# Optimization experiments

Hardware: AMD Instinct MI355X
Metric: run time of the kernel (lower is better)

The kernel has to match this reference:

```python
import jax, jax.numpy as jnp
import numpy as np

B, T, D, K = 16, 8192, 64, 1024


def setup_inputs() -> dict:
    key = jax.random.key(0)
    k1, k2 = jax.random.split(key)
    x = jax.random.normal(k1, (B, T, D, 1), dtype=jnp.float32)
    weight = jax.random.normal(k2, (K, D), dtype=jnp.float32)
    return {"x": x, "weight": weight}


def reference(x, weight):
    # x: [B, T, D, 1] -> squeeze trailing dim -> [B, T, D]
    xs = jnp.squeeze(x, axis=-1)
    x2 = jnp.sum(xs * xs, axis=-1, keepdims=True)          # [B, T, 1]
    e2 = jnp.sum(weight * weight, axis=-1)                 # [K]
    xe = jnp.einsum('btd,kd->btk', xs, weight)             # [B, T, K]
    dist2 = x2 - 2.0 * xe + e2                             # [B, T, K]
    indices = jnp.argmin(dist2, axis=-1)                   # [B, T] int
    quantized = jnp.take(weight, indices, axis=0)          # [B, T, D]
    return quantized, indices
```

## Files before the change

### kernel.cpp

```cpp
#include <hip/hip_runtime.h>

#define MTOK  131072
#define DIMD  64
#define KCODE 1024
#define TPB   128

typedef __bf16 bf16x8 __attribute__((ext_vector_type(8)));
typedef float  f32x4  __attribute__((ext_vector_type(4)));

__device__ __forceinline__ f32x4 mfma16(bf16x8 a, bf16x8 b, f32x4 c) {
    return __builtin_amdgcn_mfma_f32_16x16x32_bf16(a, b, c, 0, 0, 0);
}

__device__ __forceinline__ void g2l16(const void* g, void* l) {
    __builtin_amdgcn_global_load_lds(
        (const __attribute__((address_space(1))) unsigned int*)g,
        (__attribute__((address_space(3))) unsigned int*)l, 16, 0, 0);
}

__global__ __launch_bounds__(256) void prep_kernel(
    const float* __restrict__ w, __bf16* __restrict__ wpk,
    float* __restrict__ e2n, float* __restrict__ e2) {
    int b   = blockIdx.x;
    int tid = threadIdx.x;
    if (b < 64) {
        int cb  = b;
        int win = tid >> 6, lane = tid & 63;
        int q = lane >> 4, m = lane & 15;
        int k = cb * 16 + m;
        int d0 = (win & 1) * 32 + q * 8;
        const float* src = w + (size_t)k * DIMD + d0;
        float4 v0 = *(const float4*)(src);
        float4 v1 = *(const float4*)(src + 4);
        float f[8] = {v0.x, v0.y, v0.z, v0.w, v1.x, v1.y, v1.z, v1.w};
        bf16x8 o;
#pragma unroll
        for (int j = 0; j < 8; ++j) {
            __bf16 h = (__bf16)f[j];
            o[j] = (win < 2) ? h : (__bf16)(f[j] - (float)h);
        }
        *(bf16x8*)(wpk + ((size_t)(cb * 4 + win) * 64 + lane) * 8) = o;
    } else {
        int k2 = (b - 64) * 256 + tid;
        const float4* row = (const float4*)(w + (size_t)k2 * DIMD);
        float s = 0.f;
#pragma unroll
        for (int i = 0; i < 16; ++i) {
            float4 v = row[i];
            s = fmaf(v.x, v.x, s); s = fmaf(v.y, v.y, s);
            s = fmaf(v.z, v.z, s); s = fmaf(v.w, v.w, s);
        }
        e2[k2]  = s;
        e2n[k2] = -0.5f * s;
    }
}

__global__ __launch_bounds__(256, 4) void vq_main(
    const float* __restrict__ x, const float* __restrict__ wfull,
    const __bf16* __restrict__ wpk, const float* __restrict__ e2n_g,
    const float* __restrict__ e2_g, float* __restrict__ out) {

    __shared__ __align__(16) __bf16 ldsW[2][8192];
    __shared__ __align__(16) float  ldsE[KCODE];

    const int tid  = threadIdx.x;
    const int blk  = blockIdx.x;
    const int lane = tid & 63;
    const int wv   = tid >> 6;
    const int q    = lane >> 4;
    const int m    = lane & 15;
    const size_t tok0 = (size_t)blk * TPB + wv * 32;

    {
        const char* gw = (const char*)wpk + (size_t)wv * 4096 + (size_t)lane * 16;
        char* lw = (char*)&ldsW[0][0] + wv * 4096 + lane * 16;
#pragma unroll
        for (int j = 0; j < 4; ++j)
            g2l16(gw + j * 1024, lw + j * 1024);
        g2l16((const char*)e2n_g + (size_t)wv * 1024 + lane * 16,
              (char*)ldsE + wv * 1024 + lane * 16);
    }

    bf16x8 bx[2][4];
#pragma unroll
    for (int tg = 0; tg < 2; ++tg) {
        const float* xr = x + (tok0 + tg * 16 + m) * DIMD;
#pragma unroll
        for (int h = 0; h < 2; ++h) {
            float4 v0 = *(const float4*)(xr + h * 32 + q * 8);
            float4 v1 = *(const float4*)(xr + h * 32 + q * 8 + 4);
            float f[8] = {v0.x, v0.y, v0.z, v0.w, v1.x, v1.y, v1.z, v1.w};
            bf16x8 hi, lo;
#pragma unroll
            for (int j = 0; j < 8; ++j) {
                __bf16 hh = (__bf16)f[j];
                hi[j] = hh;
                lo[j] = (__bf16)(f[j] - (float)hh);
            }
            bx[tg][h]     = hi;
            bx[tg][2 + h] = lo;
        }
    }

    float b1[2], b2[2]; int i1[2];
#pragma unroll
    for (int tg = 0; tg < 2; ++tg) { b1[tg] = -3e38f; b2[tg] = -3e38f; i1[tg] = 0; }

    __syncthreads();

    for (int c = 0; c < 16; ++c) {
        const __bf16* wb = &ldsW[c & 1][0] + lane * 8;
        const int eb = c * 64 + q * 4;

        bf16x8 A0[2], A1[2], A2[2], A3[2];
        f32x4  EE[2];

        A0[0] = *(const bf16x8*)(wb + 0);
        A1[0] = *(const bf16x8*)(wb + 512);
        A2[0] = *(const bf16x8*)(wb + 1024);
        A3[0] = *(const bf16x8*)(wb + 1536);
        EE[0] = *(const f32x4*)&ldsE[eb];

        if (c + 1 < 16) {
            const char* gw = (const char*)wpk + (size_t)(c + 1) * 16384
                           + (size_t)wv * 4096 + (size_t)lane * 16;
            char* lw = (char*)&ldsW[(c + 1) & 1][0] + wv * 4096 + lane * 16;
#pragma unroll
            for (int j = 0; j < 4; ++j)
                g2l16(gw + j * 1024, lw + j * 1024);
        }

        A0[1] = *(const bf16x8*)(wb + 2048);
        A1[1] = *(const bf16x8*)(wb + 2048 + 512);
        A2[1] = *(const bf16x8*)(wb + 2048 + 1024);
        A3[1] = *(const bf16x8*)(wb + 2048 + 1536);
        EE[1] = *(const f32x4*)&ldsE[eb + 16];

#pragma unroll
        for (int cbl = 0; cbl < 4; ++cbl) {
            const int cur = cbl & 1;
            f32x4 t0, t1;
            __builtin_amdgcn_s_setprio(1);
            t0 = mfma16(A0[cur], bx[0][0], EE[cur]);
            t1 = mfma16(A0[cur], bx[1][0], EE[cur]);
            t0 = mfma16(A1[cur], bx[0][1], t0);
            t1 = mfma16(A1[cur], bx[1][1], t1);
            t0 = mfma16(A0[cur], bx[0][2], t0);
            t1 = mfma16(A0[cur], bx[1][2], t1);
            t0 = mfma16(A1[cur], bx[0][3], t0);
            t1 = mfma16(A1[cur], bx[1][3], t1);
            t0 = mfma16(A2[cur], bx[0][0], t0);
            t1 = mfma16(A2[cur], bx[1][0], t1);
            t0 = mfma16(A3[cur], bx[0][1], t0);
            t1 = mfma16(A3[cur], bx[1][1], t1);
            __builtin_amdgcn_s_setprio(0);

            if (cbl < 2) {
                const int nx = cbl + 2;
                A0[cur] = *(const bf16x8*)(wb + nx * 2048);
                A1[cur] = *(const bf16x8*)(wb + nx * 2048 + 512);
                A2[cur] = *(const bf16x8*)(wb + nx * 2048 + 1024);
                A3[cur] = *(const bf16x8*)(wb + nx * 2048 + 1536);
                EE[cur] = *(const f32x4*)&ldsE[eb + nx * 16];
            }

            const int cbase = (c * 4 + cbl) * 16;
#pragma unroll
            for (int r = 0; r < 4; ++r) {
                float a  = t0[r];
                int iv   = cbase + q * 4 + r;
                bool gt  = a > b1[0];
                i1[0] = gt ? iv : i1[0];
                b2[0] = __builtin_amdgcn_fmed3f(a, b1[0], b2[0]);
                b1[0] = fmaxf(a, b1[0]);
            }
#pragma unroll
            for (int r = 0; r < 4; ++r) {
                float a  = t1[r];
                int iv   = cbase + q * 4 + r;
                bool gt  = a > b1[1];
                i1[1] = gt ? iv : i1[1];
                b2[1] = __builtin_amdgcn_fmed3f(a, b1[1], b2[1]);
                b1[1] = fmaxf(a, b1[1]);
            }
        }
        if (c + 1 < 16) __syncthreads();
    }

    float B1f[2], B2f[2]; int I1f[2];
#pragma unroll
    for (int tg = 0; tg < 2; ++tg) {
        float B1 = b1[tg], B2 = b2[tg]; int I1 = i1[tg];
#pragma unroll
        for (int mask = 16; mask <= 32; mask <<= 1) {
            float ob1 = __shfl_xor(B1, mask);
            float ob2 = __shfl_xor(B2, mask);
            int   oi  = __shfl_xor(I1, mask);
            bool take = (ob1 > B1) || (ob1 == B1 && oi < I1);
            B2 = fmaxf(fminf(ob1, B1), fmaxf(ob2, B2));
            I1 = take ? oi : I1;
            B1 = fmaxf(ob1, B1);
        }
        B1f[tg] = B1; B2f[tg] = B2; I1f[tg] = I1;
    }

    int myidx;
    {
        int src = lane & 15;
        int v0 = __shfl(I1f[0], src);
        int v1 = __shfl(I1f[1], src);
        myidx = ((lane >> 4) & 1) ? v1 : v0;
    }

#pragma unroll
    for (int tg = 0; tg < 2; ++tg) {
        unsigned long long msk =
            __ballot((lane < 16) && (B1f[tg] - B2f[tg] < 2e-3f));
        while (msk) {
            int mm = __ffsll((unsigned long long)msk) - 1;
            msk &= msk - 1;
            int tloc = tg * 16 + mm;
            const float4* xr = (const float4*)(x + (tok0 + tloc) * DIMD);
            float bv = 3e38f; int bi = 0;
            for (int j = 0; j < 16; ++j) {
                int k = lane * 16 + j;
                const float4* wr = (const float4*)(wfull + (size_t)k * DIMD);
                float s = 0.f;
#pragma unroll
                for (int i = 0; i < 16; ++i) {
                    float4 xv = xr[i], wv4 = wr[i];
                    s = fmaf(xv.x, wv4.x, s); s = fmaf(xv.y, wv4.y, s);
                    s = fmaf(xv.z, wv4.z, s); s = fmaf(xv.w, wv4.w, s);
                }
                float dv = fmaf(-2.f, s, e2_g[k]);
                if (dv < bv) { bv = dv; bi = k; }
            }
#pragma unroll
            for (int mask2 = 1; mask2 <= 32; mask2 <<= 1) {
                float ov = __shfl_xor(bv, mask2);
                int   oi = __shfl_xor(bi, mask2);
                bool take = (ov < bv) || (ov == bv && oi < bi);
                bv = take ? ov : bv;
                bi = take ? oi : bi;
            }
            myidx = (lane == tloc) ? bi : myidx;
        }
    }

    if (lane < 32)
        __builtin_nontemporal_store((float)myidx,
                                    out + (size_t)MTOK * DIMD + tok0 + lane);

    {
        float* obase = out + tok0 * DIMD;
#pragma unroll
        for (int j = 0; j < 8; ++j) {
            int srcl = j * 4 + (lane >> 4);
            int gi   = __shfl(myidx, srcl);
            f32x4 v = *(const f32x4*)(wfull + (size_t)gi * DIMD + (lane & 15) * 4);
            __builtin_nontemporal_store(v, (f32x4*)(obase + j * 256 + lane * 4));
        }
    }
}

extern "C" void kernel_launch(void* const* d_in, const int* in_sizes, int n_in,
                              void* d_out, int out_size, void* d_ws, size_t ws_size,
                              hipStream_t stream) {
    const float* x = (const float*)d_in[0];
    const float* w = (const float*)d_in[1];
    float* out = (float*)d_out;

    __bf16* wpk = (__bf16*)d_ws;
    float*  e2n = (float*)((char*)d_ws + 262144);
    float*  e2  = (float*)((char*)d_ws + 266240);

    prep_kernel<<<68, 256, 0, stream>>>(w, wpk, e2n, e2);
    vq_main<<<MTOK / TPB, 256, 0, stream>>>(x, w, wpk, e2n, e2, out);
}
```

Measured before the change: 142.5 us.

## Load codebook fragments directly from global memory instead of staging through LDS

Drops the LDS double buffer for the packed bf16 codebook and the e2 norms, along with the per-chunk barriers. Each wave now reads its MFMA operand fragments straight from global memory (expected to hit L2) into registers, using a two-stage register prefetch. This removes the LDS traffic and the __syncthreads stalls. In exchange, every wave loads the whole codebook on its own, which adds global/L2 traffic and exposes higher load latency that the register prefetch may not fully hide.

Measured after the change: 153.0 us. 1.07x slower.

```diff
diff --git a/kernel.cpp b/kernel.cpp
--- a/kernel.cpp
+++ b/kernel.cpp
@@ -10,12 +10,6 @@
 
 __device__ __forceinline__ f32x4 mfma16(bf16x8 a, bf16x8 b, f32x4 c) {
     return __builtin_amdgcn_mfma_f32_16x16x32_bf16(a, b, c, 0, 0, 0);
-}
-
-__device__ __forceinline__ void g2l16(const void* g, void* l) {
-    __builtin_amdgcn_global_load_lds(
-        (const __attribute__((address_space(1))) unsigned int*)g,
-        (__attribute__((address_space(3))) unsigned int*)l, 16, 0, 0);
 }
 
 __global__ __launch_bounds__(256) void prep_kernel(
@@ -60,9 +54,6 @@
     const __bf16* __restrict__ wpk, const float* __restrict__ e2n_g,
     const float* __restrict__ e2_g, float* __restrict__ out) {
 
-    __shared__ __align__(16) __bf16 ldsW[2][8192];
-    __shared__ __align__(16) float  ldsE[KCODE];
-
     const int tid  = threadIdx.x;
     const int blk  = blockIdx.x;
     const int lane = tid & 63;
@@ -71,16 +62,6 @@
     const int m    = lane & 15;
     const size_t tok0 = (size_t)blk * TPB + wv * 32;
 
-    {
-        const char* gw = (const char*)wpk + (size_t)wv * 4096 + (size_t)lane * 16;
-        char* lw = (char*)&ldsW[0][0] + wv * 4096 + lane * 16;
-#pragma unroll
-        for (int j = 0; j < 4; ++j)
-            g2l16(gw + j * 1024, lw + j * 1024);
-        g2l16((const char*)e2n_g + (size_t)wv * 1024 + lane * 16,
-              (char*)ldsE + wv * 1024 + lane * 16);
-    }
-
     bf16x8 bx[2][4];
 #pragma unroll
     for (int tg = 0; tg < 2; ++tg) {
@@ -106,85 +87,76 @@
 #pragma unroll
     for (int tg = 0; tg < 2; ++tg) { b1[tg] = -3e38f; b2[tg] = -3e38f; i1[tg] = 0; }
 
-    __syncthreads();
-
-    for (int c = 0; c < 16; ++c) {
-        const __bf16* wb = &ldsW[c & 1][0] + lane * 8;
-        const int eb = c * 64 + q * 4;
-
-        bf16x8 A0[2], A1[2], A2[2], A3[2];
-        f32x4  EE[2];
-
-        A0[0] = *(const bf16x8*)(wb + 0);
-        A1[0] = *(const bf16x8*)(wb + 512);
-        A2[0] = *(const bf16x8*)(wb + 1024);
-        A3[0] = *(const bf16x8*)(wb + 1536);
-        EE[0] = *(const f32x4*)&ldsE[eb];
-
-        if (c + 1 < 16) {
-            const char* gw = (const char*)wpk + (size_t)(c + 1) * 16384
-                           + (size_t)wv * 4096 + (size_t)lane * 16;
-            char* lw = (char*)&ldsW[(c + 1) & 1][0] + wv * 4096 + lane * 16;
-#pragma unroll
-            for (int j = 0; j < 4; ++j)
-                g2l16(gw + j * 1024, lw + j * 1024);
-        }
-
-        A0[1] = *(const bf16x8*)(wb + 2048);
-        A1[1] = *(const bf16x8*)(wb + 2048 + 512);
-        A2[1] = *(const bf16x8*)(wb + 2048 + 1024);
-        A3[1] = *(const bf16x8*)(wb + 2048 + 1536);
-        EE[1] = *(const f32x4*)&ldsE[eb + 16];
-
-#pragma unroll
-        for (int cbl = 0; cbl < 4; ++cbl) {
-            const int cur = cbl & 1;
-            f32x4 t0, t1;
-            __builtin_amdgcn_s_setprio(1);
-            t0 = mfma16(A0[cur], bx[0][0], EE[cur]);
-            t1 = mfma16(A0[cur], bx[1][0], EE[cur]);
-            t0 = mfma16(A1[cur], bx[0][1], t0);
-            t1 = mfma16(A1[cur], bx[1][1], t1);
-            t0 = mfma16(A0[cur], bx[0][2], t0);
-            t1 = mfma16(A0[cur], bx[1][2], t1);
-            t0 = mfma16(A1[cur], bx[0][3], t0);
-            t1 = mfma16(A1[cur], bx[1][3], t1);
-            t0 = mfma16(A2[cur], bx[0][0], t0);
-            t1 = mfma16(A2[cur], bx[1][0], t1);
-            t0 = mfma16(A3[cur], bx[0][1], t0);
-            t1 = mfma16(A3[cur], bx[1][1], t1);
-            __builtin_amdgcn_s_setprio(0);
-
-            if (cbl < 2) {
-                const int nx = cbl + 2;
-                A0[cur] = *(const bf16x8*)(wb + nx * 2048);
-                A1[cur] = *(const bf16x8*)(wb + nx * 2048 + 512);
-                A2[cur] = *(const bf16x8*)(wb + nx * 2048 + 1024);
-                A3[cur] = *(const bf16x8*)(wb + nx * 2048 + 1536);
-                EE[cur] = *(const f32x4*)&ldsE[eb + nx * 16];
-            }
-
-            const int cbase = (c * 4 + cbl) * 16;
-#pragma unroll
-            for (int r = 0; r < 4; ++r) {
-                float a  = t0[r];
-                int iv   = cbase + q * 4 + r;
-                bool gt  = a > b1[0];
-                i1[0] = gt ? iv : i1[0];
-                b2[0] = __builtin_amdgcn_fmed3f(a, b1[0], b2[0]);
-                b1[0] = fmaxf(a, b1[0]);
-            }
-#pragma unroll
-            for (int r = 0; r < 4; ++r) {
-                float a  = t1[r];
-                int iv   = cbase + q * 4 + r;
-                bool gt  = a > b1[1];
-                i1[1] = gt ? iv : i1[1];
-                b2[1] = __builtin_amdgcn_fmed3f(a, b1[1], b2[1]);
-                b1[1] = fmaxf(a, b1[1]);
-            }
-        }
-        if (c + 1 < 16) __syncthreads();
+    const __bf16* wp = wpk + (size_t)lane * 8;
+    const float*  ep = e2n_g + q * 4;
+
+    auto compute = [&](const bf16x8& A0, const bf16x8& A1, const bf16x8& A2,
+                       const bf16x8& A3, const f32x4& EE, int cbase) {
+        __builtin_amdgcn_s_setprio(1);
+        f32x4 t0 = mfma16(A0, bx[0][0], EE);
+        f32x4 t1 = mfma16(A0, bx[1][0], EE);
+        t0 = mfma16(A1, bx[0][1], t0);
+        t1 = mfma16(A1, bx[1][1], t1);
+        t0 = mfma16(A0, bx[0][2], t0);
+        t1 = mfma16(A0, bx[1][2], t1);
+        t0 = mfma16(A1, bx[0][3], t0);
+        t1 = mfma16(A1, bx[1][3], t1);
+        t0 = mfma16(A2, bx[0][0], t0);
+        t1 = mfma16(A2, bx[1][0], t1);
+        t0 = mfma16(A3, bx[0][1], t0);
+        t1 = mfma16(A3, bx[1][1], t1);
+        __builtin_amdgcn_s_setprio(0);
+#pragma unroll
+        for (int r = 0; r < 4; ++r) {
+            float a  = t0[r];
+            int iv   = cbase + q * 4 + r;
+            bool gt  = a > b1[0];
+            i1[0] = gt ? iv : i1[0];
+            b2[0] = __builtin_amdgcn_fmed3f(a, b1[0], b2[0]);
+            b1[0] = fmaxf(a, b1[0]);
+        }
+#pragma unroll
+        for (int r = 0; r < 4; ++r) {
+            float a  = t1[r];
+            int iv   = cbase + q * 4 + r;
+            bool gt  = a > b1[1];
+            i1[1] = gt ? iv : i1[1];
+            b2[1] = __builtin_amdgcn_fmed3f(a, b1[1], b2[1]);
+            b1[1] = fmaxf(a, b1[1]);
+        }
+    };
+
+    bf16x8 Pa0, Pa1, Pa2, Pa3, Pb0, Pb1, Pb2, Pb3;
+    f32x4  Ea, Eb;
+
+    {
+        const __bf16* wc = wp;
+        Pa0 = *(const bf16x8*)(wc + 0);
+        Pa1 = *(const bf16x8*)(wc + 512);
+        Pa2 = *(const bf16x8*)(wc + 1024);
+        Pa3 = *(const bf16x8*)(wc + 1536);
+        Ea  = *(const f32x4*)(ep);
+    }
+
+    for (int cb = 0; cb < 64; cb += 2) {
+        {
+            const __bf16* wc = wp + (size_t)(cb + 1) * 2048;
+            Pb0 = *(const bf16x8*)(wc + 0);
+            Pb1 = *(const bf16x8*)(wc + 512);
+            Pb2 = *(const bf16x8*)(wc + 1024);
+            Pb3 = *(const bf16x8*)(wc + 1536);
+            Eb  = *(const f32x4*)(ep + (cb + 1) * 16);
+        }
+        compute(Pa0, Pa1, Pa2, Pa3, Ea, cb * 16);
+        if (cb + 2 < 64) {
+            const __bf16* wc = wp + (size_t)(cb + 2) * 2048;
+            Pa0 = *(const bf16x8*)(wc + 0);
+            Pa1 = *(const bf16x8*)(wc + 512);
+            Pa2 = *(const bf16x8*)(wc + 1024);
+            Pa3 = *(const bf16x8*)(wc + 1536);
+            Ea  = *(const f32x4*)(ep + (cb + 2) * 16);
+        }
+        compute(Pb0, Pb1, Pb2, Pb3, Eb, (cb + 1) * 16);
     }
 
     float B1f[2], B2f[2]; int I1f[2];
```
